# Kernel optimization log

Hardware: AMD Instinct MI355X
Metric: run time of the kernel (lower is better)

Reference implementation:

```python
import jax, jax.numpy as jnp
import numpy as np

N = 4096      # nodes
E = 131072    # edges (before self loops)
C = 512       # channels
H = 8         # heads
CO = C // H   # per-head out channels (64)
EPS = 1e-5
NEG_SLOPE = 0.2


def layer_norm(x, g, b):
    mu = jnp.mean(x, axis=-1, keepdims=True)
    var = jnp.mean((x - mu) ** 2, axis=-1, keepdims=True)
    return (x - mu) * jax.lax.rsqrt(var + EPS) * g + b


def gatv2(x, src, dst, wl, bl, wr, br, att, bias):
    # PyG GATv2Conv, concat=True, add_self_loops handled by caller.
    n = x.shape[0]
    xl = (x @ wl.T + bl).reshape(n, H, CO)   # target-side features
    xr = (x @ wr.T + br).reshape(n, H, CO)   # source-side features (messages)
    e = jax.nn.leaky_relu(xl[dst] + xr[src], NEG_SLOPE)   # [E+N, H, CO]
    alpha = jnp.einsum('ehc,hc->eh', e, att)              # [E+N, H]
    # segment softmax over destination neighborhoods
    amax = jax.ops.segment_max(alpha, dst, num_segments=n)
    ex = jnp.exp(alpha - amax[dst])
    denom = jax.ops.segment_sum(ex, dst, num_segments=n)
    a = ex / denom[dst]                                   # [E+N, H]
    msg = xr[src] * a[:, :, None]                         # [E+N, H, CO]
    out = jax.ops.segment_sum(msg, dst, num_segments=n)   # [N, H, CO]
    return out.reshape(n, H * CO) + bias


def mha(x, in_w, in_b, out_w, out_b):
    # nn.MultiheadAttention self-attention, batch=1, eval mode
    n = x.shape[0]
    qkv = x @ in_w.T + in_b                               # [N, 3C]
    q, k, v = jnp.split(qkv, 3, axis=-1)
    q = q.reshape(n, H, CO); k = k.reshape(n, H, CO); v = v.reshape(n, H, CO)
    scores = jnp.einsum('qhd,khd->hqk', q, k) / jnp.sqrt(jnp.float32(CO))
    p = jax.nn.softmax(scores, axis=-1)
    o = jnp.einsum('hqk,khd->qhd', p, v).reshape(n, C)
    return o @ out_w.T + out_b


def setup_inputs() -> dict:
    key = jax.random.key(0)
    ks = jax.random.split(key, 24)
    s = 0.02
    d = {}
    d['x'] = jax.random.normal(ks[0], (N, C), jnp.float32)
    d['edge_index'] = jax.random.randint(ks[1], (2, E), 0, N, dtype=jnp.int64)
    d['gat_wl'] = jax.random.normal(ks[2], (H * CO, C), jnp.float32) * s
    d['gat_bl'] = jnp.zeros((H * CO,), jnp.float32)
    d['gat_wr'] = jax.random.normal(ks[3], (H * CO, C), jnp.float32) * s
    d['gat_br'] = jnp.zeros((H * CO,), jnp.float32)
    d['gat_att'] = jax.random.normal(ks[4], (H, CO), jnp.float32) * s
    d['gat_b'] = jnp.zeros((H * CO,), jnp.float32)
    d['in_w'] = jax.random.normal(ks[5], (3 * C, C), jnp.float32) * s
    d['in_b'] = jnp.zeros((3 * C,), jnp.float32)
    d['out_w'] = jax.random.normal(ks[6], (C, C), jnp.float32) * s
    d['out_b'] = jnp.zeros((C,), jnp.float32)
    d['ln1_g'] = jnp.ones((C,), jnp.float32); d['ln1_b'] = jnp.zeros((C,), jnp.float32)
    d['ln2_g'] = jnp.ones((C,), jnp.float32); d['ln2_b'] = jnp.zeros((C,), jnp.float32)
    d['ln3_g'] = jnp.ones((C,), jnp.float32); d['ln3_b'] = jnp.zeros((C,), jnp.float32)
    d['w1'] = jax.random.normal(ks[7], (4 * C, C), jnp.float32) * s
    d['b1'] = jnp.zeros((4 * C,), jnp.float32)
    d['w2'] = jax.random.normal(ks[8], (C, 4 * C), jnp.float32) * s
    d['b2'] = jnp.zeros((C,), jnp.float32)
    return d


def reference(x, edge_index, gat_wl, gat_bl, gat_wr, gat_br, gat_att, gat_b,
              in_w, in_b, out_w, out_b, ln1_g, ln1_b, ln2_g, ln2_b,
              ln3_g, ln3_b, w1, b1, w2, b2):
    n = x.shape[0]
    loops = jnp.arange(n, dtype=edge_index.dtype)
    src = jnp.concatenate([edge_index[0], loops])
    dst = jnp.concatenate([edge_index[1], loops])
    h_local = gatv2(x, src, dst, gat_wl, gat_bl, gat_wr, gat_br, gat_att, gat_b)
    x = layer_norm(x + h_local, ln1_g, ln1_b)
    h_global = mha(x, in_w, in_b, out_w, out_b)
    x = layer_norm(x + h_global, ln2_g, ln2_b)
    h_ffn = (jax.nn.gelu(x @ w1.T + b1, approximate=False)) @ w2.T + b2
    x = layer_norm(x + h_ffn, ln3_g, ln3_b)
    return x
```

## Files before the change

### kernel.cpp

```cpp
#include <hip/hip_runtime.h>
#include <math.h>

#define NN 4096
#define CC 512
#define EE 131072
#define NEDGE (EE + NN)
#define HH 8
#define DCO 64
#define NC2 2097152L

typedef __attribute__((ext_vector_type(8))) short bfrag;
typedef __attribute__((ext_vector_type(4))) float f32x4;
typedef __attribute__((ext_vector_type(4))) int i32x4;

__device__ __forceinline__ float bf2f(unsigned short u) {
  union { float f; unsigned int i; } x; x.i = ((unsigned int)u) << 16; return x.f;
}
__device__ __forceinline__ unsigned short f2bf(float f) {
  union { float f; unsigned int i; } x; x.f = f;
  unsigned int r = x.i + 0x7FFFu + ((x.i >> 16) & 1u);
  return (unsigned short)(r >> 16);
}
__device__ __forceinline__ unsigned short f2bf_trunc(float f) {
  union { float f; unsigned int i; } x; x.f = f;
  return (unsigned short)(x.i >> 16);
}

__device__ __forceinline__ void gld16(const unsigned short* g, unsigned short* l) {
  __builtin_amdgcn_global_load_lds(
      (__attribute__((address_space(1))) unsigned int*)g,
      (__attribute__((address_space(3))) unsigned int*)l, 16, 0, 0);
}

#define QSC 0.18033688011112042f

#define CX  2097152L
#define CWL (CX + 262144L)
#define CWR (CWL + 262144L)
#define CIW (CWR + 786432L)
#define COW (CIW + 262144L)
#define CW1 (COW + 1048576L)
#define CW2 (CW1 + 1048576L)

__global__ void cvt_all(const float* __restrict__ x, const float* __restrict__ wl,
                        const float* __restrict__ wr, const float* __restrict__ iw,
                        const float* __restrict__ ow, const float* __restrict__ w1,
                        const float* __restrict__ w2, unsigned short* __restrict__ dst,
                        int* __restrict__ cntcur, const float* __restrict__ bl,
                        const float* __restrict__ br, float* __restrict__ biasc) {
  if (blockIdx.x >= 5632) {
    int t = threadIdx.x;
    if (blockIdx.x == 5632) {
      for (int k = t; k < 8192; k += 256) cntcur[k] = 0;
    } else {
      for (int k = t; k < 512; k += 256) {
        biasc[k] = bl[k];
        biasc[512 + k] = br[k];
      }
    }
    return;
  }
  long i = ((long)blockIdx.x * 256 + threadIdx.x) * 4;
  const float* s; long o;
  if (i < CX)       { s = x;  o = i; }
  else if (i < CWL) { s = wl; o = i - CX; }
  else if (i < CWR) { s = wr; o = i - CWL; }
  else if (i < CIW) { s = iw; o = i - CWR; }
  else if (i < COW) { s = ow; o = i - CIW; }
  else if (i < CW1) { s = w1; o = i - COW; }
  else              { s = w2; o = i - CW1; }
  f32x4 v = *(const f32x4*)(s + o);
  union { unsigned long long q; unsigned short u[4]; } t;
#pragma unroll
  for (int j = 0; j < 4; j++) t.u[j] = f2bf(v[j]);
  *(unsigned long long*)(dst + i) = t.q;
}

template<int OMODE, int TN, bool SPLIT>
__global__ __launch_bounds__(256) void gemm_t(
    const unsigned short* __restrict__ A, const unsigned short* __restrict__ B,
    const float* __restrict__ bias, void* __restrict__ C,
    int K, int lda, int ldb, int ldc)
{
  __shared__ unsigned short As[4096];
  __shared__ unsigned short Bs[TN * 32];
  constexpr int MI = (TN == 128) ? 4 : 2;
  const int tid = threadIdx.x;
  const int wave = tid >> 6, lane = tid & 63;
  const int ml = lane & 15, kq = lane >> 4;
  const int wm = (TN == 128) ? ((wave >> 1) << 6) : (wave << 5);
  const int wn = (TN == 128) ? ((wave & 1) << 6) : 0;
  const int bm = blockIdx.y << 7, bn = blockIdx.x * TN;
  const int srow = tid >> 2, scol = (tid & 3) << 3;
  if (SPLIT) { A += (long)blockIdx.z * K; B += (long)blockIdx.z * K; }
  const float* biasp = (!SPLIT || blockIdx.z == 0) ? bias : nullptr;
  const unsigned short* Ag = A + (long)(bm + srow) * lda + scol;
  const unsigned short* Bg = B + (long)(bn + srow) * ldb + scol;
  const long astep = (long)64 * lda, bstep = (long)64 * ldb;
  unsigned short* lA0 = As + tid * 8;
  unsigned short* lA1 = As + 2048 + tid * 8;
  unsigned short* lB0 = Bs + tid * 8;
  f32x4 acc[MI][4];
#pragma unroll
  for (int mi = 0; mi < MI; mi++)
#pragma unroll
    for (int ni = 0; ni < 4; ni++) acc[mi][ni] = (f32x4){0.f, 0.f, 0.f, 0.f};
  for (int k0 = 0; k0 < K; k0 += 32) {
    __syncthreads();
    gld16(Ag, lA0); gld16(Ag + astep, lA1);
    gld16(Bg, lB0);
    if (TN == 128) gld16(Bg + bstep, Bs + 2048 + tid * 8);
    Ag += 32; Bg += 32;
    __syncthreads();
    bfrag af[MI], bf[4];
#pragma unroll
    for (int mi = 0; mi < MI; mi++)
      af[mi] = *(const bfrag*)&As[(wm + (mi << 4) + ml) * 32 + (kq << 3)];
#pragma unroll
    for (int ni = 0; ni < 4; ni++)
      bf[ni] = *(const bfrag*)&Bs[(wn + (ni << 4) + ml) * 32 + (kq << 3)];
#pragma unroll
    for (int mi = 0; mi < MI; mi++)
#pragma unroll
      for (int ni = 0; ni < 4; ni++)
        acc[mi][ni] = __builtin_amdgcn_mfma_f32_16x16x32_bf16(af[mi], bf[ni], acc[mi][ni], 0, 0, 0);
  }
#pragma unroll
  for (int ni = 0; ni < 4; ni++) {
    int col = bn + wn + (ni << 4) + ml;
    float bb = biasp ? biasp[col] : 0.f;
#pragma unroll
    for (int mi = 0; mi < MI; mi++) {
      int row0 = bm + wm + (mi << 4) + (kq << 2);
#pragma unroll
      for (int r = 0; r < 4; r++) {
        float v = acc[mi][ni][r] + bb;
        int row = row0 + r;
        if (OMODE == 3) {
          unsigned short* q = (unsigned short*)C;
          if (col < 512) {
            int h = col >> 6, d = col & 63;
            q[(long)h * (NN * DCO) + (long)row * DCO + d] = f2bf(v * QSC);
          } else if (col < 1024) {
            int c2 = col - 512, h = c2 >> 6, d = c2 & 63;
            q[NC2 + (long)h * (NN * DCO) + (long)row * DCO + d] = f2bf(v);
          } else {
            int c2 = col - 1024, h = c2 >> 6, d = c2 & 63;
            q[2 * NC2 + (long)h * (DCO * NN) + (long)d * NN + row] = f2bf(v);
          }
        } else if (OMODE == 0) {
          long off = (SPLIT ? (long)blockIdx.z * NC2 : 0) + (long)row * ldc + col;
          ((float*)C)[off] = v;
        } else {
          if (OMODE == 2) v = 0.5f * v * (1.f + erff(v * 0.70710678118f));
          ((unsigned short*)C)[(long)row * ldc + col] = f2bf(v);
        }
      }
    }
  }
}

__global__ void count_k(const int* __restrict__ ei, int* __restrict__ cnt) {
  int e = blockIdx.x * 256 + threadIdx.x;
  if (e >= NEDGE) return;
  int d = (e < EE) ? ei[EE + e] : (e - EE);
  atomicAdd(&cnt[d], 1);
}

__global__ void scan_k(const int* __restrict__ cnt, int* __restrict__ rowptr) {
  __shared__ int s[1024];
  int t = threadIdx.x;
  int b = t * 4;
  int c0 = cnt[b], c1 = cnt[b + 1], c2 = cnt[b + 2], c3 = cnt[b + 3];
  int sum = c0 + c1 + c2 + c3;
  s[t] = sum;
  __syncthreads();
  for (int o = 1; o < 1024; o <<= 1) {
    int v = (t >= o) ? s[t - o] : 0;
    __syncthreads();
    s[t] += v;
    __syncthreads();
  }
  int ex = s[t] - sum;
  rowptr[b] = ex; rowptr[b + 1] = ex + c0;
  rowptr[b + 2] = ex + c0 + c1; rowptr[b + 3] = ex + c0 + c1 + c2;
  if (t == 1023) rowptr[4096] = ex + sum;
}

__global__ void scatter_k(const int* __restrict__ ei, const int* __restrict__ rowptr,
                          int* __restrict__ cur, int* __restrict__ order) {
  int e = blockIdx.x * 256 + threadIdx.x;
  if (e >= NEDGE) return;
  int d = (e < EE) ? ei[EE + e] : (e - EE);
  int p = atomicAdd(&cur[d], 1);
  order[rowptr[d] + p] = e;
}

__global__ __launch_bounds__(256) void gat_fused(
    const unsigned short* __restrict__ xlr, const float* __restrict__ x,
    const int* __restrict__ order, const int* __restrict__ rowptr,
    const int* __restrict__ ei, const float* __restrict__ att,
    const float* __restrict__ gbias,
    const float* __restrict__ g, const float* __restrict__ be,
    float* __restrict__ of, unsigned short* __restrict__ ob)
{
  __shared__ float part[4][512];
  __shared__ float sw[4][8];
  __shared__ float sinv[8];
  __shared__ float shl[8];
  int n = blockIdx.x, t = threadIdx.x;
  int beg = rowptr[n], deg = rowptr[n + 1] - beg;
  int wave = t >> 6, lane = t & 63;
  int ch = lane << 3;
  union U8 { i32x4 v; unsigned short u[8]; };
  U8 XL; XL.v = *(const i32x4*)(xlr + (long)n * 1024 + ch);
  float xl[8];
#pragma unroll
  for (int j = 0; j < 8; j++) xl[j] = bf2f(XL.u[j]);
  f32x4 t0 = *(const f32x4*)(att + ch);
  f32x4 t1 = *(const f32x4*)(att + ch + 4);
  float acc[8];
#pragma unroll
  for (int j = 0; j < 8; j++) acc[j] = 0.f;
  float se = 0.f;
  int i = wave;
  U8 X;
  if (i < deg) {
    int e = order[beg + i];
    int sn = (e < EE) ? ei[e] : (e - EE);
    X.v = *(const i32x4*)(xlr + (long)sn * 1024 + 512 + ch);
  }
  while (i < deg) {
    U8 Xc = X;
    int inext = i + 4;
    if (inext < deg) {
      int e = order[beg + inext];
      int sn = (e < EE) ? ei[e] : (e - EE);
      X.v = *(const i32x4*)(xlr + (long)sn * 1024 + 512 + ch);
    }
    float xr[8];
    float p = 0.f;
#pragma unroll
    for (int j = 0; j < 8; j++) {
      xr[j] = bf2f(Xc.u[j]);
      float v = xl[j] + xr[j];
      v = (v > 0.f) ? v : 0.2f * v;
      float tv = (j < 4) ? t0[j] : t1[j - 4];
      p += tv * v;
    }
    p += __shfl_xor(p, 1); p += __shfl_xor(p, 2); p += __shfl_xor(p, 4);
    float ew = __expf(p);
    se += ew;
#pragma unroll
    for (int j = 0; j < 8; j++) acc[j] += ew * xr[j];
    i = inext;
  }
  *(f32x4*)&part[wave][ch]     = (f32x4){acc[0], acc[1], acc[2], acc[3]};
  *(f32x4*)&part[wave][ch + 4] = (f32x4){acc[4], acc[5], acc[6], acc[7]};
  if ((lane & 7) == 0) sw[wave][lane >> 3] = se;
  __syncthreads();
  if (t < 8) sinv[t] = 1.f / (sw[0][t] + sw[1][t] + sw[2][t] + sw[3][t]);
  __syncthreads();
  long base = (long)n * CC;
  float v0, v1;
  {
    int c = t;
    float p4 = part[0][c] + part[1][c] + part[2][c] + part[3][c];
    v0 = x[base + c] + p4 * sinv[c >> 6] + gbias[c];
  }
  {
    int c = t + 256;
    float p4 = part[0][c] + part[1][c] + part[2][c] + part[3][c];
    v1 = x[base + c] + p4 * sinv[c >> 6] + gbias[c];
  }
  float s = v0 + v1, ss = v0 * v0 + v1 * v1;
  for (int o = 32; o > 0; o >>= 1) { s += __shfl_down(s, o); ss += __shfl_down(ss, o); }
  if (lane == 0) { shl[wave] = s; shl[4 + wave] = ss; }
  __syncthreads();
  float S = shl[0] + shl[1] + shl[2] + shl[3];
  float SS = shl[4] + shl[5] + shl[6] + shl[7];
  float mean = S * (1.f / 512.f);
  float var = SS * (1.f / 512.f) - mean * mean;
  float rs = rsqrtf(var + 1e-5f);
  float y0 = (v0 - mean) * rs * g[t] + be[t];
  float y1 = (v1 - mean) * rs * g[t + 256] + be[t + 256];
  of[base + t] = y0; of[base + t + 256] = y1;
  ob[base + t] = f2bf(y0); ob[base + t + 256] = f2bf(y1);
}

template<int NS>
__global__ __launch_bounds__(256) void resid_ln(
    const float* __restrict__ a, const float* __restrict__ b,
    const float* __restrict__ g, const float* __restrict__ be,
    float* __restrict__ of, unsigned short* __restrict__ ob)
{
  __shared__ float sh[8];
  int row = blockIdx.x, t = threadIdx.x;
  long base = (long)row * CC;
  float b0 = 0.f, b1 = 0.f;
#pragma unroll
  for (int s = 0; s < NS; s++) {
    b0 += b[(long)s * NC2 + base + t];
    b1 += b[(long)s * NC2 + base + t + 256];
  }
  float v0 = a[base + t] + b0;
  float v1 = a[base + t + 256] + b1;
  float s = v0 + v1, ss = v0 * v0 + v1 * v1;
  for (int o = 32; o > 0; o >>= 1) { s += __shfl_down(s, o); ss += __shfl_down(ss, o); }
  int wave = t >> 6, lane = t & 63;
  if (lane == 0) { sh[wave] = s; sh[4 + wave] = ss; }
  __syncthreads();
  float S = sh[0] + sh[1] + sh[2] + sh[3];
  float SS = sh[4] + sh[5] + sh[6] + sh[7];
  float mean = S * (1.f / 512.f);
  float var = SS * (1.f / 512.f) - mean * mean;
  float rs = rsqrtf(var + 1e-5f);
  float y0 = (v0 - mean) * rs * g[t] + be[t];
  float y1 = (v1 - mean) * rs * g[t + 256] + be[t + 256];
  if (of) { of[base + t] = y0; of[base + t + 256] = y1; }
  if (ob) { ob[base + t] = f2bf(y0); ob[base + t + 256] = f2bf(y1); }
}

__global__ __launch_bounds__(256, 4) void flash_attn(
    const unsigned short* __restrict__ qkvP, unsigned short* __restrict__ Op,
    float* __restrict__ Lp)
{
  __shared__ unsigned short QP[128 * 72];
  __shared__ unsigned short Ks[64 * 72];
  __shared__ unsigned short Vs[64 * 72];
  const int tid = threadIdx.x;
  const int wave = tid >> 6, lane = tid & 63;
  const int ml = lane & 15, kq = lane >> 4;
  const int h = blockIdx.x & 7, qt = blockIdx.x >> 3;
  const int sp = blockIdx.y;
  const int n0 = qt << 7;
  const unsigned short* Qh = qkvP + (long)h * (NN * DCO);
  const unsigned short* Kh = qkvP + NC2 + (long)h * (NN * DCO);
  const unsigned short* Vh = qkvP + 2 * NC2 + (long)h * (DCO * NN);
  {
    int r = tid >> 1, c = (tid & 1) << 5;
    const unsigned short* src = Qh + (long)(n0 + r) * DCO + c;
    unsigned short* d = &QP[r * 72 + c];
    *(i32x4*)d        = *(const i32x4*)src;
    *(i32x4*)(d + 8)  = *(const i32x4*)(src + 8);
    *(i32x4*)(d + 16) = *(const i32x4*)(src + 16);
    *(i32x4*)(d + 24) = *(const i32x4*)(src + 24);
  }
  __syncthreads();
  bfrag aq[2][2];
#pragma unroll
  for (int s = 0; s < 2; s++)
#pragma unroll
    for (int kh = 0; kh < 2; kh++)
      aq[s][kh] = *(const bfrag*)&QP[(wave * 32 + s * 16 + ml) * 72 + kh * 32 + (kq << 3)];
  bfrag ones;
#pragma unroll
  for (int j = 0; j < 8; j++) ones[j] = (short)0x3F80;
  f32x4 Oa[2][4];
  f32x4 Lc[2];
#pragma unroll
  for (int s = 0; s < 2; s++) {
    Lc[s] = (f32x4){0.f, 0.f, 0.f, 0.f};
#pragma unroll
    for (int dg = 0; dg < 4; dg++) Oa[s][dg] = (f32x4){0.f, 0.f, 0.f, 0.f};
  }
  const int r_ = tid >> 2, c_ = (tid & 3) << 4;
  const int j0 = sp << 4;
  i32x4 ka, kb, va, vb;
  {
    int k0 = j0 << 6;
    ka = *(const i32x4*)(Kh + (long)(k0 + r_) * DCO + c_);
    kb = *(const i32x4*)(Kh + (long)(k0 + r_) * DCO + c_ + 8);
    va = *(const i32x4*)(Vh + (long)r_ * NN + k0 + c_);
    vb = *(const i32x4*)(Vh + (long)r_ * NN + k0 + c_ + 8);
  }
  for (int jj = 0; jj < 16; jj++) {
    if (jj) __syncthreads();
    *(i32x4*)&Ks[r_ * 72 + c_] = ka; *(i32x4*)&Ks[r_ * 72 + c_ + 8] = kb;
    *(i32x4*)&Vs[r_ * 72 + c_] = va; *(i32x4*)&Vs[r_ * 72 + c_ + 8] = vb;
    __syncthreads();
    if (jj < 15) {
      int k0 = (j0 + jj + 1) << 6;
      ka = *(const i32x4*)(Kh + (long)(k0 + r_) * DCO + c_);
      kb = *(const i32x4*)(Kh + (long)(k0 + r_) * DCO + c_ + 8);
      va = *(const i32x4*)(Vh + (long)r_ * NN + k0 + c_);
      vb = *(const i32x4*)(Vh + (long)r_ * NN + k0 + c_ + 8);
    }
    f32x4 sc[2][4];
#pragma unroll
    for (int s = 0; s < 2; s++)
#pragma unroll
      for (int c = 0; c < 4; c++) sc[s][c] = (f32x4){0.f, 0.f, 0.f, 0.f};
    __builtin_amdgcn_s_setprio(1);
#pragma unroll
    for (int c = 0; c < 4; c++) {
      bfrag bk0 = *(const bfrag*)&Ks[(c * 16 + ml) * 72 + (kq << 3)];
      bfrag bk1 = *(const bfrag*)&Ks[(c * 16 + ml) * 72 + 32 + (kq << 3)];
#pragma unroll
      for (int s = 0; s < 2; s++) {
        sc[s][c] = __builtin_amdgcn_mfma_f32_16x16x32_bf16(bk0, aq[s][0], sc[s][c], 0, 0, 0);
        sc[s][c] = __builtin_amdgcn_mfma_f32_16x16x32_bf16(bk1, aq[s][1], sc[s][c], 0, 0, 0);
      }
    }
    __builtin_amdgcn_s_setprio(0);
#pragma unroll
    for (int s = 0; s < 2; s++) {
#pragma unroll
      for (int c = 0; c < 4; c++) {
        unsigned int w0, w1;
        float e0, e1, e2, e3;
        asm("v_exp_f32 %2, %6\n\t"
            "v_exp_f32 %3, %7\n\t"
            "v_exp_f32 %4, %8\n\t"
            "v_exp_f32 %5, %9\n\t"
            "v_cvt_pk_bf16_f32 %0, %2, %3\n\t"
            "v_cvt_pk_bf16_f32 %1, %4, %5"
            : "=v"(w0), "=v"(w1), "=&v"(e0), "=&v"(e1), "=&v"(e2), "=&v"(e3)
            : "v"(sc[s][c][0]), "v"(sc[s][c][1]), "v"(sc[s][c][2]), "v"(sc[s][c][3]));
        union { unsigned long long q; unsigned int w[2]; } u;
        u.w[0] = w0; u.w[1] = w1;
        *(unsigned long long*)&QP[(wave * 32 + s * 16 + ml) * 72 + c * 16 + (kq << 2)] = u.q;
      }
    }
    bfrag ap[2][2];
#pragma unroll
    for (int s = 0; s < 2; s++)
#pragma unroll
      for (int kh = 0; kh < 2; kh++)
        ap[s][kh] = *(const bfrag*)&QP[(wave * 32 + s * 16 + ml) * 72 + kh * 32 + (kq << 3)];
    __builtin_amdgcn_s_setprio(1);
#pragma unroll
    for (int s = 0; s < 2; s++) {
      Lc[s] = __builtin_amdgcn_mfma_f32_16x16x32_bf16(ap[s][0], ones, Lc[s], 0, 0, 0);
      Lc[s] = __builtin_amdgcn_mfma_f32_16x16x32_bf16(ap[s][1], ones, Lc[s], 0, 0, 0);
    }
#pragma unroll
    for (int dg = 0; dg < 4; dg++) {
      bfrag bv0 = *(const bfrag*)&Vs[(dg * 16 + ml) * 72 + (kq << 3)];
      bfrag bv1 = *(const bfrag*)&Vs[(dg * 16 + ml) * 72 + 32 + (kq << 3)];
#pragma unroll
      for (int s = 0; s < 2; s++) {
        Oa[s][dg] = __builtin_amdgcn_mfma_f32_16x16x32_bf16(ap[s][0], bv0, Oa[s][dg], 0, 0, 0);
        Oa[s][dg] = __builtin_amdgcn_mfma_f32_16x16x32_bf16(ap[s][1], bv1, Oa[s][dg], 0, 0, 0);
      }
    }
    __builtin_amdgcn_s_setprio(0);
  }
  long obase = (long)sp * NC2;
#pragma unroll
  for (int s = 0; s < 2; s++)
#pragma unroll
    for (int dg = 0; dg < 4; dg++)
#pragma unroll
      for (int r = 0; r < 4; r++) {
        int row = wave * 32 + s * 16 + (kq << 2) + r;
        Op[obase + (long)(n0 + row) * CC + (h << 6) + (dg << 4) + ml] = f2bf(Oa[s][dg][r]);
      }
  if (ml == 0) {
#pragma unroll
    for (int s = 0; s < 2; s++)
#pragma unroll
      for (int r = 0; r < 4; r++) {
        int row = wave * 32 + s * 16 + (kq << 2) + r;
        Lp[(long)sp * (NN * HH) + (long)(n0 + row) * HH + h] = Lc[s][r];
      }
  }
}

__global__ void flash_combine(const unsigned short* __restrict__ Op,
                              const float* __restrict__ Lp,
                              unsigned short* __restrict__ Ao) {
  int idx = blockIdx.x * 256 + threadIdx.x;
  int n = idx >> 9, c = idx & 511, h = c >> 6;
  float l = 0.f, o = 0.f;
#pragma unroll
  for (int s = 0; s < 4; s++) {
    l += Lp[(long)s * (NN * HH) + (long)n * HH + h];
    o += bf2f(Op[(long)s * NC2 + idx]);
  }
  Ao[idx] = f2bf(o / l);
}

extern "C" void kernel_launch(void* const* d_in, const int* in_sizes, int n_in,
                              void* d_out, int out_size, void* d_ws, size_t ws_size,
                              hipStream_t stream) {
  typedef unsigned short u16;
  const float* x      = (const float*)d_in[0];
  const int*   ei     = (const int*)d_in[1];
  const float* wl     = (const float*)d_in[2];
  const float* bl     = (const float*)d_in[3];
  const float* wr     = (const float*)d_in[4];
  const float* br     = (const float*)d_in[5];
  const float* att    = (const float*)d_in[6];
  const float* gat_b  = (const float*)d_in[7];
  const float* in_w   = (const float*)d_in[8];
  const float* in_b   = (const float*)d_in[9];
  const float* out_w  = (const float*)d_in[10];
  const float* out_b  = (const float*)d_in[11];
  const float* ln1g   = (const float*)d_in[12];
  const float* ln1b   = (const float*)d_in[13];
  const float* ln2g   = (const float*)d_in[14];
  const float* ln2b   = (const float*)d_in[15];
  const float* ln3g   = (const float*)d_in[16];
  const float* ln3b   = (const float*)d_in[17];
  const float* w1     = (const float*)d_in[18];
  const float* b1     = (const float*)d_in[19];
  const float* w2     = (const float*)d_in[20];
  const float* b2     = (const float*)d_in[21];

  const size_t MB = 1u << 20;
  char* w = (char*)d_ws;
  float* h_f32   = (float*)(w + 0);
  float* x2_f32  = (float*)(w + 8 * MB);
  int*   cnt     = (int*)(w + 16 * MB);
  int*   cur     = cnt + 4096;
  int*   rowptr  = (int*)(w + 16 * MB + 32 * 1024);
  int*   order   = (int*)(w + 16 * MB + 64 * 1024);
  u16*   cvt     = (u16*)(w + 17 * MB);
  u16*   xbf     = cvt;
  u16*   wlrbf   = cvt + CX;
  u16*   inwbf   = cvt + CWR;
  u16*   outwbf  = cvt + CIW;
  u16*   w1bf    = cvt + COW;
  u16*   w2bf    = cvt + CW1;
  u16*   xlr_bf  = (u16*)(w + 29 * MB);
  u16*   Opart   = (u16*)(w + 29 * MB);
  float* proj    = (float*)(w + 29 * MB);
  u16*   ffn1    = (u16*)(w + 61 * MB);
  u16*   qkvP    = (u16*)(w + 93 * MB);
  float* biasc   = (float*)(w + 105 * MB);
  float* Lpart   = (float*)(w + 105 * MB);
  u16*   Ao      = (u16*)(w + 106 * MB);
  u16*   actb    = (u16*)(w + 110 * MB);

  cvt_all<<<5634, 256, 0, stream>>>(x, wl, wr, in_w, out_w, w1, w2, cvt,
                                    cnt, bl, br, biasc);
  count_k<<<(NEDGE + 255) / 256, 256, 0, stream>>>(ei, cnt);
  scan_k<<<1, 1024, 0, stream>>>(cnt, rowptr);
  scatter_k<<<(NEDGE + 255) / 256, 256, 0, stream>>>(ei, rowptr, cur, order);

  gemm_t<1, 64, false><<<dim3(16, 32), 256, 0, stream>>>(xbf, wlrbf, biasc, xlr_bf, 512, 512, 512, 1024);
  gat_fused<<<NN, 256, 0, stream>>>(xlr_bf, x, order, rowptr, ei, att, gat_b,
                                    ln1g, ln1b, h_f32, actb);

  gemm_t<3, 64, false><<<dim3(24, 32), 256, 0, stream>>>(actb, inwbf, in_b, qkvP, 512, 512, 512, 0);
  flash_attn<<<dim3(256, 4), 256, 0, stream>>>(qkvP, Opart, Lpart);
  flash_combine<<<(NN * CC) / 256, 256, 0, stream>>>(Opart, Lpart, Ao);
  gemm_t<0, 64, true><<<dim3(8, 32, 2), 256, 0, stream>>>(Ao, outwbf, out_b, proj, 256, 512, 512, 512);
  resid_ln<2><<<NN, 256, 0, stream>>>(h_f32, proj, ln2g, ln2b, x2_f32, actb);

  gemm_t<2, 64, false><<<dim3(32, 32), 256, 0, stream>>>(actb, w1bf, b1, ffn1, 512, 512, 512, 2048);
  gemm_t<0, 64, true><<<dim3(8, 32, 4), 256, 0, stream>>>(ffn1, w2bf, b2, proj, 512, 2048, 2048, 512);
  resid_ln<4><<<NN, 256, 0, stream>>>(x2_f32, proj, ln3g, ln3b, (float*)d_out, nullptr);
}
```

Baseline: 312.3 us.

## Replace block GEMM with single-wave 32x64 tiles and triple-buffered async loads

Swaps the 256-thread 128x64 GEMM for a single-wave kernel that computes 32x64 tiles. Global-to-LDS loads are triple-buffered and gated with explicit vmcnt waits instead of __syncthreads. The aim is to remove block-wide barriers, overlap loads with MFMA, and launch four times as many blocks for better occupancy. The cost is less reuse of A and B per block, so global and L2 traffic goes up, and correctness now depends on the exact count of outstanding vm loads.

```diff
diff --git a/kernel.cpp b/kernel.cpp
--- a/kernel.cpp
+++ b/kernel.cpp
@@ -76,62 +76,75 @@
   *(unsigned long long*)(dst + i) = t.q;
 }
 
-template<int OMODE, int TN, bool SPLIT>
-__global__ __launch_bounds__(256) void gemm_t(
+template<int OMODE, bool SPLIT>
+__global__ __launch_bounds__(64) void gemm_w(
     const unsigned short* __restrict__ A, const unsigned short* __restrict__ B,
     const float* __restrict__ bias, void* __restrict__ C,
     int K, int lda, int ldb, int ldc)
 {
-  __shared__ unsigned short As[4096];
-  __shared__ unsigned short Bs[TN * 32];
-  constexpr int MI = (TN == 128) ? 4 : 2;
-  const int tid = threadIdx.x;
-  const int wave = tid >> 6, lane = tid & 63;
-  const int ml = lane & 15, kq = lane >> 4;
-  const int wm = (TN == 128) ? ((wave >> 1) << 6) : (wave << 5);
-  const int wn = (TN == 128) ? ((wave & 1) << 6) : 0;
-  const int bm = blockIdx.y << 7, bn = blockIdx.x * TN;
-  const int srow = tid >> 2, scol = (tid & 3) << 3;
+  __shared__ unsigned short As[3 * 1024];
+  __shared__ unsigned short Bs[3 * 2048];
+  const int l = threadIdx.x;
+  const int ml = l & 15, kq = l >> 4;
+  const int bm = blockIdx.y << 5, bn = blockIdx.x << 6;
   if (SPLIT) { A += (long)blockIdx.z * K; B += (long)blockIdx.z * K; }
   const float* biasp = (!SPLIT || blockIdx.z == 0) ? bias : nullptr;
-  const unsigned short* Ag = A + (long)(bm + srow) * lda + scol;
-  const unsigned short* Bg = B + (long)(bn + srow) * ldb + scol;
-  const long astep = (long)64 * lda, bstep = (long)64 * ldb;
-  unsigned short* lA0 = As + tid * 8;
-  unsigned short* lA1 = As + 2048 + tid * 8;
-  unsigned short* lB0 = Bs + tid * 8;
-  f32x4 acc[MI][4];
-#pragma unroll
-  for (int mi = 0; mi < MI; mi++)
+  const int rq = l >> 2, cq = (l & 3) << 3;
+  const unsigned short* Ag = A + (long)(bm + rq) * lda + cq;
+  const unsigned short* Bg = B + (long)(bn + rq) * ldb + cq;
+  const long a16 = 16L * lda, b16 = 16L * ldb;
+  f32x4 acc[2][4];
+#pragma unroll
+  for (int mi = 0; mi < 2; mi++)
 #pragma unroll
     for (int ni = 0; ni < 4; ni++) acc[mi][ni] = (f32x4){0.f, 0.f, 0.f, 0.f};
-  for (int k0 = 0; k0 < K; k0 += 32) {
-    __syncthreads();
-    gld16(Ag, lA0); gld16(Ag + astep, lA1);
-    gld16(Bg, lB0);
-    if (TN == 128) gld16(Bg + bstep, Bs + 2048 + tid * 8);
-    Ag += 32; Bg += 32;
-    __syncthreads();
-    bfrag af[MI], bf[4];
-#pragma unroll
-    for (int mi = 0; mi < MI; mi++)
-      af[mi] = *(const bfrag*)&As[(wm + (mi << 4) + ml) * 32 + (kq << 3)];
+  const int nt = K >> 5;
+#define STAGE_W(tt, bb) do {                                   \
+    const unsigned short* sa_ = Ag + (tt) * 32;                \
+    const unsigned short* sb_ = Bg + (tt) * 32;                \
+    gld16(sa_,            As + (bb) * 1024 + l * 8);           \
+    gld16(sa_ + a16,      As + (bb) * 1024 + 512 + l * 8);     \
+    gld16(sb_,            Bs + (bb) * 2048 + l * 8);           \
+    gld16(sb_ + b16,      Bs + (bb) * 2048 + 512 + l * 8);     \
+    gld16(sb_ + 2 * b16,  Bs + (bb) * 2048 + 1024 + l * 8);    \
+    gld16(sb_ + 3 * b16,  Bs + (bb) * 2048 + 1536 + l * 8);    \
+  } while (0)
+  STAGE_W(0, 0);
+  STAGE_W(1, 1);
+  int cur = 0;
+  for (int t = 0; t < nt; t++) {
+    if (t + 2 < nt) {
+      int sbuf = cur + 2; if (sbuf >= 3) sbuf -= 3;
+      STAGE_W(t + 2, sbuf);
+    }
+    int fl = nt - 1 - t; if (fl > 2) fl = 2;
+    if (fl == 2)      asm volatile("s_waitcnt vmcnt(12)" ::: "memory");
+    else if (fl == 1) asm volatile("s_waitcnt vmcnt(6)" ::: "memory");
+    else              asm volatile("s_waitcnt vmcnt(0)" ::: "memory");
+    const unsigned short* Ab = As + cur * 1024;
+    const unsigned short* Bb = Bs + cur * 2048;
+    bfrag af[2], bf[4];
+#pragma unroll
+    for (int mi = 0; mi < 2; mi++)
+      af[mi] = *(const bfrag*)&Ab[((mi << 4) + ml) * 32 + (kq << 3)];
 #pragma unroll
     for (int ni = 0; ni < 4; ni++)
-      bf[ni] = *(const bfrag*)&Bs[(wn + (ni << 4) + ml) * 32 + (kq << 3)];
-#pragma unroll
-    for (int mi = 0; mi < MI; mi++)
+      bf[ni] = *(const bfrag*)&Bb[((ni << 4) + ml) * 32 + (kq << 3)];
+#pragma unroll
+    for (int mi = 0; mi < 2; mi++)
 #pragma unroll
       for (int ni = 0; ni < 4; ni++)
         acc[mi][ni] = __builtin_amdgcn_mfma_f32_16x16x32_bf16(af[mi], bf[ni], acc[mi][ni], 0, 0, 0);
-  }
+    cur++; if (cur == 3) cur = 0;
+  }
+#undef STAGE_W
 #pragma unroll
   for (int ni = 0; ni < 4; ni++) {
-    int col = bn + wn + (ni << 4) + ml;
+    int col = bn + (ni << 4) + ml;
     float bb = biasp ? biasp[col] : 0.f;
 #pragma unroll
-    for (int mi = 0; mi < MI; mi++) {
-      int row0 = bm + wm + (mi << 4) + (kq << 2);
+    for (int mi = 0; mi < 2; mi++) {
+      int row0 = bm + (mi << 4) + (kq << 2);
 #pragma unroll
       for (int r = 0; r < 4; r++) {
         float v = acc[mi][ni][r] + bb;
@@ -539,17 +552,17 @@
   scan_k<<<1, 1024, 0, stream>>>(cnt, rowptr);
   scatter_k<<<(NEDGE + 255) / 256, 256, 0, stream>>>(ei, rowptr, cur, order);
 
-  gemm_t<1, 64, false><<<dim3(16, 32), 256, 0, stream>>>(xbf, wlrbf, biasc, xlr_bf, 512, 512, 512, 1024);
+  gemm_w<1, false><<<dim3(16, 128), 64, 0, stream>>>(xbf, wlrbf, biasc, xlr_bf, 512, 512, 512, 1024);
   gat_fused<<<NN, 256, 0, stream>>>(xlr_bf, x, order, rowptr, ei, att, gat_b,
                                     ln1g, ln1b, h_f32, actb);
 
-  gemm_t<3, 64, false><<<dim3(24, 32), 256, 0, stream>>>(actb, inwbf, in_b, qkvP, 512, 512, 512, 0);
+  gemm_w<3, false><<<dim3(24, 128), 64, 0, stream>>>(actb, inwbf, in_b, qkvP, 512, 512, 512, 0);
   flash_attn<<<dim3(256, 4), 256, 0, stream>>>(qkvP, Opart, Lpart);
   flash_combine<<<(NN * CC) / 256, 256, 0, stream>>>(Opart, Lpart, Ao);
-  gemm_t<0, 64, true><<<dim3(8, 32, 2), 256, 0, stream>>>(Ao, outwbf, out_b, proj, 256, 512, 512, 512);
+  gemm_w<0, true><<<dim3(8, 128, 2), 64, 0, stream>>>(Ao, outwbf, out_b, proj, 256, 512, 512, 512);
   resid_ln<2><<<NN, 256, 0, stream>>>(h_f32, proj, ln2g, ln2b, x2_f32, actb);
 
-  gemm_t<2, 64, false><<<dim3(32, 32), 256, 0, stream>>>(actb, w1bf, b1, ffn1, 512, 512, 512, 2048);
-  gemm_t<0, 64, true><<<dim3(8, 32, 4), 256, 0, stream>>>(ffn1, w2bf, b2, proj, 512, 2048, 2048, 512);
+  gemm_w<2, false><<<dim3(32, 128), 64, 0, stream>>>(actb, w1bf, b1, ffn1, 512, 512, 512, 2048);
+  gemm_w<0, true><<<dim3(8, 128, 4), 64, 0, stream>>>(ffn1, w2bf, b2, proj, 512, 2048, 2048, 512);
   resid_ln<4><<<NN, 256, 0, stream>>>(x2_f32, proj, ln3g, ln3b, (float*)d_out, nullptr);
 }
```

New measurement: 335.9 us. 1.08x slower.
